# Kernel optimization log

Measured on AMD Instinct MI355X. Metric: run time of the kernel, lower is better.

Reference implementation:

```python
import jax, jax.numpy as jnp
import numpy as np

B, S, D, R, N_IN, N_PROC, K = 4, 4096, 1024, 128, 8, 32, 4

def setup_inputs() -> dict:
    key = jax.random.key(0)
    k1, k2, k3, k4, k5 = jax.random.split(key, 5)
    x = jax.random.normal(k1, (B, S, D), dtype=jnp.float32)
    input_weights = jax.random.uniform(k2, (B, S, N_IN), dtype=jnp.float32)
    process_indices = jax.random.randint(k3, (B, S, K), 0, N_PROC, dtype=jnp.int32)
    # params: orthogonal-ish init approximated by scaled gaussian
    input_neurons = jax.random.normal(k4, (N_IN, D, R), dtype=jnp.float32) / np.sqrt(D).astype(np.float32)
    process_neurons = jax.random.normal(k5, (N_PROC, R), dtype=jnp.float32)
    process_neurons = process_neurons / (jnp.linalg.norm(process_neurons, axis=-1, keepdims=True) + 1e-8)
    return {"x": x, "input_weights": input_weights, "process_indices": process_indices,
            "input_neurons": input_neurons, "process_neurons": process_neurons}

def reference(x, input_weights, process_indices, input_neurons, process_neurons):
    # soft routing over input neurons: project with all N_IN matrices, weight, sum
    all_proj = jnp.einsum('bsd,ndr->bsnr', x, input_neurons)      # [B,S,N_IN,R]
    y = jnp.einsum('bsnr,bsn->bsr', all_proj, input_weights)       # [B,S,R]
    # gather per-token Householder vectors: [B,S,K,R]
    selected_v = process_neurons[process_indices]
    # sequential chain of K Householder reflections via scan over the K axis
    def step(xc, v):
        # v: [B,S,R]
        v_norm_sq = jnp.sum(v * v, axis=-1, keepdims=True) + 1e-8
        vn = v / jnp.sqrt(v_norm_sq)
        vTx = jnp.sum(xc * vn, axis=-1, keepdims=True)
        return xc - 2.0 * vn * vTx, None
    out, _ = jax.lax.scan(step, y, jnp.moveaxis(selected_v, 2, 0))
    return out
```

## Files before the change

### kernel.cpp

```cpp
#include <hip/hip_runtime.h>
#include <hip/hip_bf16.h>
#include <stdint.h>

#define D_DIM 1024
#define R_DIM 128
#define NIN   8
#define M_TOT 16384

typedef unsigned short u16;
typedef __attribute__((ext_vector_type(4))) float f32x4;
typedef __attribute__((ext_vector_type(8))) __bf16 bf16x8;

__device__ __forceinline__ u16 f2b(float f) {
    union { float f; uint32_t u; } v; v.f = f;
    uint32_t r = (v.u + 0x7FFFu + ((v.u >> 16) & 1u)) >> 16;
    return (u16)r;
}

__device__ __forceinline__ void gload16(const void* g, void* l) {
    __builtin_amdgcn_global_load_lds(
        (const __attribute__((address_space(1))) uint32_t*)g,
        (__attribute__((address_space(3))) uint32_t*)l, 16, 0, 0);
}

#define SBAR do { asm volatile("" ::: "memory"); __builtin_amdgcn_s_barrier(); asm volatile("" ::: "memory"); } while (0)
#define WVM4 asm volatile("s_waitcnt vmcnt(4)" ::: "memory")

__global__ __launch_bounds__(256)
void prep(const float* __restrict__ x, u16* __restrict__ xb,
          const float* __restrict__ inn, u16* __restrict__ Bt2) {
    if (blockIdx.x < 8192) {
        const size_t i = ((size_t)blockIdx.x * 256 + threadIdx.x) * 8;
        const f32x4 v0 = *(const f32x4*)&x[i];
        const f32x4 v1 = *(const f32x4*)&x[i + 4];
        union { u16 s[8]; uint4 v; } u;
#pragma unroll
        for (int q = 0; q < 4; ++q) { u.s[q] = f2b(v0[q]); u.s[4 + q] = f2b(v1[q]); }
        *(uint4*)&xb[i] = u.v;
    } else {
        const int idx = (int)blockIdx.x - 8192;
        const int n  = idx >> 4;
        const int d0 = (idx & 15) * 64;
        const int r   = threadIdx.x & 127;
        const int hf  = threadIdx.x >> 7;
        const size_t C = (size_t)((r >> 4) * 128 + n * 16 + (r & 15));
#pragma unroll
        for (int g = 0; g < 4; ++g) {
            const int gg = hf * 4 + g;
            union { u16 s[8]; uint4 v; } u;
#pragma unroll
            for (int jj = 0; jj < 8; ++jj)
                u.s[jj] = f2b(inn[((size_t)n * D_DIM + d0 + gg * 8 + jj) * R_DIM + r]);
            *(uint4*)&Bt2[C * D_DIM + d0 + gg * 8] = u.v;
        }
    }
}

__global__ __launch_bounds__(512, 2)
void gemm8(const u16* __restrict__ xb, const u16* __restrict__ Bt2,
           const float* __restrict__ iw, float* __restrict__ y) {
    __shared__ __align__(16) char smem[131072];
    char* As = smem;
    char* Bs = smem + 65536;

    const int tid  = threadIdx.x;
    const int wid  = tid >> 6, lane = tid & 63;
    const int wm = wid >> 2, wn = wid & 3;
    const int l15 = lane & 15, lq = lane >> 4;

    int wg = (int)blockIdx.x;
    wg = (wg & 7) * 32 + (wg >> 3);
    const int by = wg & 3, bx = wg >> 2;
    const int m0 = bx * 256, c0 = by * 256;

    const int sxor = ((tid & 7) * 16) ^ (((tid >> 3) & 7) << 4);
    const char* gA = (const char*)xb  + ((size_t)(m0 + (tid >> 3))) * 2048 + sxor;
    const char* gB = (const char*)Bt2 + ((size_t)(c0 + (tid >> 3))) * 2048 + sxor;

#define STA(T1, NB, Q) gload16(gA + (size_t)(Q) * 64 * 2048 + (size_t)(T1) * 128, As + (NB) * 32768 + (Q) * 8192 + tid * 16)
#define STB(T1, NB, C) gload16(gB + (size_t)(C) * 64 * 2048 + (size_t)(T1) * 128, Bs + (NB) * 32768 + (C) * 8192 + tid * 16)

#define RDA(DST, MH, CUR) \
    _Pragma("unroll") for (int i = 0; i < 4; ++i) \
    _Pragma("unroll") for (int kk = 0; kk < 2; ++kk) { \
        const int row = wm * 128 + (MH) * 64 + i * 16 + l15; \
        uint32_t off = (uint32_t)((CUR) * 32768 + row * 128 + kk * 64 + lq * 16); \
        off ^= (uint32_t)((row & 7) << 4); \
        DST[i][kk] = *(const bf16x8*)(As + off); }

#define RDB(NS, CUR) \
    _Pragma("unroll") for (int j = 0; j < 2; ++j) \
    _Pragma("unroll") for (int kk = 0; kk < 2; ++kk) { \
        const int cc = (NS) * 128 + wn * 32 + j * 16 + l15; \
        uint32_t off = (uint32_t)((CUR) * 32768 + cc * 128 + kk * 64 + lq * 16); \
        off ^= (uint32_t)((cc & 7) << 4); \
        b[NS][j][kk] = *(const bf16x8*)(Bs + off); }

#define MM(MH, NS, AF) do { \
    __builtin_amdgcn_s_setprio(1); \
    _Pragma("unroll") for (int i = 0; i < 4; ++i) \
    _Pragma("unroll") for (int j = 0; j < 2; ++j) \
    _Pragma("unroll") for (int kk = 0; kk < 2; ++kk) \
        acc[MH][NS][i][j] = __builtin_amdgcn_mfma_f32_16x16x32_bf16(AF[i][kk], b[NS][j][kk], acc[MH][NS][i][j], 0, 0, 0); \
    __builtin_amdgcn_s_setprio(0); } while (0)

    f32x4 acc[2][2][4][2] = {};

    STA(0, 0, 0); STA(0, 0, 2);
    STB(0, 0, 0); STB(0, 0, 1);
    STB(0, 0, 2); STB(0, 0, 3);
    STA(0, 0, 1); STA(0, 0, 3);
    WVM4; SBAR;

    for (int t = 0; t < 16; ++t) {
        const int cur = t & 1, nb = cur ^ 1;
        const int t1 = t + 1;
        const bool st = (t1 < 16);
        bf16x8 a0[4][2], a1[4][2], b[2][2][2];

        RDA(a0, 0, cur);
        RDB(0, cur);
        if (st) { STA(t1, nb, 0); STA(t1, nb, 2); }
        SBAR;
        MM(0, 0, a0);
        WVM4; SBAR;

        RDB(1, cur);
        if (st) { STB(t1, nb, 0); STB(t1, nb, 1); }
        SBAR;
        MM(0, 1, a0);
        WVM4; SBAR;

        RDA(a1, 1, cur);
        if (st) { STB(t1, nb, 2); STB(t1, nb, 3); }
        SBAR;
        MM(1, 0, a1);
        SBAR;

        if (st) { STA(t1, nb, 1); STA(t1, nb, 3); }
        SBAR;
        MM(1, 1, a1);
        WVM4; SBAR;
    }

    float* P0 = (float*)smem;
    float* P1 = (float*)(smem + 34816);
    const float* wrow = iw + (size_t)m0 * NIN;

    float own[2][2][4][4];
#pragma unroll
    for (int mh = 0; mh < 2; ++mh)
#pragma unroll
        for (int i = 0; i < 4; ++i)
#pragma unroll
            for (int e = 0; e < 4; ++e) {
                const int row = wm * 128 + mh * 64 + i * 16 + lq * 4 + e;
                const float w0 = wrow[row * NIN + wn * 2 + 0];
                const float w1 = wrow[row * NIN + wn * 2 + 1];
#pragma unroll
                for (int ns = 0; ns < 2; ++ns)
                    own[mh][ns][i][e] = w0 * acc[mh][ns][i][0][e] + w1 * acc[mh][ns][i][1][e];
            }

#define PIX(NS, ROW) ((NS) * (256 * 17) + (ROW) * 17 + l15)
    if (wn == 1 || wn == 3) {
        float* P = (wn == 1) ? P0 : P1;
#pragma unroll
        for (int mh = 0; mh < 2; ++mh)
#pragma unroll
            for (int ns = 0; ns < 2; ++ns)
#pragma unroll
                for (int i = 0; i < 4; ++i)
#pragma unroll
                    for (int e = 0; e < 4; ++e) {
                        const int row = wm * 128 + mh * 64 + i * 16 + lq * 4 + e;
                        P[PIX(ns, row)] = own[mh][ns][i][e];
                    }
    }
    SBAR;
    if (wn == 2) {
#pragma unroll
        for (int mh = 0; mh < 2; ++mh)
#pragma unroll
            for (int ns = 0; ns < 2; ++ns)
#pragma unroll
                for (int i = 0; i < 4; ++i)
#pragma unroll
                    for (int e = 0; e < 4; ++e) {
                        const int row = wm * 128 + mh * 64 + i * 16 + lq * 4 + e;
                        P1[PIX(ns, row)] += own[mh][ns][i][e];
                    }
    }
    SBAR;
    if (wn == 0) {
#pragma unroll
        for (int mh = 0; mh < 2; ++mh)
#pragma unroll
            for (int ns = 0; ns < 2; ++ns)
#pragma unroll
                for (int i = 0; i < 4; ++i)
#pragma unroll
                    for (int e = 0; e < 4; ++e) {
                        const int row = wm * 128 + mh * 64 + i * 16 + lq * 4 + e;
                        const float s = own[mh][ns][i][e] + P0[PIX(ns, row)] + P1[PIX(ns, row)];
                        y[(size_t)(m0 + row) * R_DIM + (2 * by + ns) * 16 + l15] = s;
                    }
    }
#undef PIX
#undef MM
#undef RDB
#undef RDA
#undef STB
#undef STA
}

__global__ __launch_bounds__(512)
void house(float* __restrict__ y, const int* __restrict__ pidx,
           const float* __restrict__ pn) {
    const int tid = threadIdx.x;
    const int row = tid >> 3;
    const int cg  = tid & 7;
    const int c0  = cg * 16;
    const int tok = blockIdx.x * 64 + row;

    float yv[16];
#pragma unroll
    for (int q = 0; q < 4; ++q) {
        const f32x4 s = *(const f32x4*)&y[(size_t)tok * R_DIM + c0 + q * 4];
        yv[q * 4 + 0] = s[0]; yv[q * 4 + 1] = s[1]; yv[q * 4 + 2] = s[2]; yv[q * 4 + 3] = s[3];
    }

    const int4 idx4 = *(const int4*)&pidx[tok * 4];
    const int idxs[4] = { idx4.x, idx4.y, idx4.z, idx4.w };

#pragma unroll
    for (int k = 0; k < 4; ++k) {
        const float* vptr = &pn[(size_t)idxs[k] * R_DIM + c0];
        float v[16];
#pragma unroll
        for (int q = 0; q < 4; ++q) {
            const f32x4 vv4 = *(const f32x4*)&vptr[q * 4];
            v[q * 4 + 0] = vv4[0]; v[q * 4 + 1] = vv4[1];
            v[q * 4 + 2] = vv4[2]; v[q * 4 + 3] = vv4[3];
        }
        float vy = 0.f, vv = 0.f;
#pragma unroll
        for (int j = 0; j < 16; ++j) { vy += v[j] * yv[j]; vv += v[j] * v[j]; }
#pragma unroll
        for (int o = 1; o < 8; o <<= 1) {
            vy += __shfl_xor(vy, o);
            vv += __shfl_xor(vv, o);
        }
        const float s = 2.0f * vy / (vv + 1e-8f);
#pragma unroll
        for (int j = 0; j < 16; ++j) yv[j] -= s * v[j];
    }

#pragma unroll
    for (int q = 0; q < 4; ++q) {
        f32x4 o; o[0] = yv[q*4+0]; o[1] = yv[q*4+1]; o[2] = yv[q*4+2]; o[3] = yv[q*4+3];
        *(f32x4*)&y[(size_t)tok * R_DIM + c0 + q * 4] = o;
    }
}

extern "C" void kernel_launch(void* const* d_in, const int* in_sizes, int n_in,
                              void* d_out, int out_size, void* d_ws, size_t ws_size,
                              hipStream_t stream) {
    const float* x   = (const float*)d_in[0];
    const float* iw  = (const float*)d_in[1];
    const int*   pix = (const int*)d_in[2];
    const float* inn = (const float*)d_in[3];
    const float* pn  = (const float*)d_in[4];
    float* out = (float*)d_out;

    u16* xb  = (u16*)d_ws;
    u16* Bt2 = (u16*)((char*)d_ws + (size_t)(32 << 20));

    prep<<<8320, 256, 0, stream>>>(x, xb, inn, Bt2);
    gemm8<<<256, 512, 0, stream>>>(xb, Bt2, iw, out);
    house<<<256, 512, 0, stream>>>(out, pix, pn);
}
```

Measured before the change: 66.35 us.

## Fuse x fp32-to-bf16 conversion into GEMM A-tile loading

Removes the separate prep pass that converted x to bf16 in a workspace. The GEMM now loads fp32 x straight into registers, converts it, and writes the swizzled bf16 tile into LDS, with the pipeline rescheduled around the new waits. This avoids writing and re-reading a 32MB intermediate, but doubles the A-side global bytes each GEMM block reads and adds register pressure and conversion work inside the main loop.

```diff
diff --git a/kernel.cpp b/kernel.cpp
--- a/kernel.cpp
+++ b/kernel.cpp
@@ -23,41 +23,31 @@
         (__attribute__((address_space(3))) uint32_t*)l, 16, 0, 0);
 }
 
-#define SBAR do { asm volatile("" ::: "memory"); __builtin_amdgcn_s_barrier(); asm volatile("" ::: "memory"); } while (0)
-#define WVM4 asm volatile("s_waitcnt vmcnt(4)" ::: "memory")
+#define SBAR  do { asm volatile("" ::: "memory"); __builtin_amdgcn_s_barrier(); asm volatile("" ::: "memory"); } while (0)
+#define SBARL do { asm volatile("s_waitcnt lgkmcnt(0)" ::: "memory"); __builtin_amdgcn_s_barrier(); asm volatile("" ::: "memory"); } while (0)
+#define WVMC(N) asm volatile("s_waitcnt vmcnt(" #N ")" ::: "memory")
 
 __global__ __launch_bounds__(256)
-void prep(const float* __restrict__ x, u16* __restrict__ xb,
-          const float* __restrict__ inn, u16* __restrict__ Bt2) {
-    if (blockIdx.x < 8192) {
-        const size_t i = ((size_t)blockIdx.x * 256 + threadIdx.x) * 8;
-        const f32x4 v0 = *(const f32x4*)&x[i];
-        const f32x4 v1 = *(const f32x4*)&x[i + 4];
+void prep_b(const float* __restrict__ inn, u16* __restrict__ Bt2) {
+    const int idx = (int)blockIdx.x;
+    const int n  = idx >> 4;
+    const int d0 = (idx & 15) * 64;
+    const int r   = threadIdx.x & 127;
+    const int hf  = threadIdx.x >> 7;
+    const size_t C = (size_t)((r >> 4) * 128 + n * 16 + (r & 15));
+#pragma unroll
+    for (int g = 0; g < 4; ++g) {
+        const int gg = hf * 4 + g;
         union { u16 s[8]; uint4 v; } u;
 #pragma unroll
-        for (int q = 0; q < 4; ++q) { u.s[q] = f2b(v0[q]); u.s[4 + q] = f2b(v1[q]); }
-        *(uint4*)&xb[i] = u.v;
-    } else {
-        const int idx = (int)blockIdx.x - 8192;
-        const int n  = idx >> 4;
-        const int d0 = (idx & 15) * 64;
-        const int r   = threadIdx.x & 127;
-        const int hf  = threadIdx.x >> 7;
-        const size_t C = (size_t)((r >> 4) * 128 + n * 16 + (r & 15));
-#pragma unroll
-        for (int g = 0; g < 4; ++g) {
-            const int gg = hf * 4 + g;
-            union { u16 s[8]; uint4 v; } u;
-#pragma unroll
-            for (int jj = 0; jj < 8; ++jj)
-                u.s[jj] = f2b(inn[((size_t)n * D_DIM + d0 + gg * 8 + jj) * R_DIM + r]);
-            *(uint4*)&Bt2[C * D_DIM + d0 + gg * 8] = u.v;
-        }
+        for (int jj = 0; jj < 8; ++jj)
+            u.s[jj] = f2b(inn[((size_t)n * D_DIM + d0 + gg * 8 + jj) * R_DIM + r]);
+        *(uint4*)&Bt2[C * D_DIM + d0 + gg * 8] = u.v;
     }
 }
 
 __global__ __launch_bounds__(512, 2)
-void gemm8(const u16* __restrict__ xb, const u16* __restrict__ Bt2,
+void gemm8(const float* __restrict__ x, const u16* __restrict__ Bt2,
            const float* __restrict__ iw, float* __restrict__ y) {
     __shared__ __align__(16) char smem[131072];
     char* As = smem;
@@ -73,12 +63,33 @@
     const int by = wg & 3, bx = wg >> 2;
     const int m0 = bx * 256, c0 = by * 256;
 
+    const int arow = tid >> 3;
+    const int slot = tid & 7;
+    const uint32_t awoff = (uint32_t)(arow * 128 + ((slot * 16) ^ ((arow & 7) << 4)));
+    const float* pAq[4];
+#pragma unroll
+    for (int Q = 0; Q < 4; ++Q)
+        pAq[Q] = x + (size_t)(m0 + Q * 64 + arow) * D_DIM + slot * 8;
+
     const int sxor = ((tid & 7) * 16) ^ (((tid >> 3) & 7) << 4);
-    const char* gA = (const char*)xb  + ((size_t)(m0 + (tid >> 3))) * 2048 + sxor;
     const char* gB = (const char*)Bt2 + ((size_t)(c0 + (tid >> 3))) * 2048 + sxor;
 
-#define STA(T1, NB, Q) gload16(gA + (size_t)(Q) * 64 * 2048 + (size_t)(T1) * 128, As + (NB) * 32768 + (Q) * 8192 + tid * 16)
 #define STB(T1, NB, C) gload16(gB + (size_t)(C) * 64 * 2048 + (size_t)(T1) * 128, Bs + (NB) * 32768 + (C) * 8192 + tid * 16)
+
+#define LDAG(AR, T1) do { \
+    const size_t ko_ = (size_t)(T1) * 64; \
+    _Pragma("unroll") for (int Q = 0; Q < 4; ++Q) { \
+        AR[Q][0] = *(const f32x4*)(pAq[Q] + ko_); \
+        AR[Q][1] = *(const f32x4*)(pAq[Q] + ko_ + 4); } \
+} while (0)
+
+#define WRA(AR, NB) do { \
+    _Pragma("unroll") for (int Q = 0; Q < 4; ++Q) { \
+        bf16x8 v8_; \
+        _Pragma("unroll") for (int j = 0; j < 4; ++j) { \
+            v8_[j] = (__bf16)AR[Q][0][j]; v8_[4 + j] = (__bf16)AR[Q][1][j]; } \
+        *(bf16x8*)(As + (NB) * 32768 + Q * 8192 + awoff) = v8_; } \
+} while (0)
 
 #define RDA(DST, MH, CUR) \
     _Pragma("unroll") for (int i = 0; i < 4; ++i) \
@@ -104,43 +115,38 @@
         acc[MH][NS][i][j] = __builtin_amdgcn_mfma_f32_16x16x32_bf16(AF[i][kk], b[NS][j][kk], acc[MH][NS][i][j], 0, 0, 0); \
     __builtin_amdgcn_s_setprio(0); } while (0)
 
+#define TILE(T, CUR, NB) do { \
+    const int t1_ = (T) + 1; const bool st_ = (t1_ < 16); \
+    bf16x8 a0[4][2], a1[4][2], b[2][2][2]; \
+    f32x4 ar[4][2]; \
+    RDA(a0, 0, CUR); RDB(0, CUR); \
+    if (st_) LDAG(ar, t1_); \
+    SBAR; MM(0, 0, a0); \
+    if (st_) { WVMC(8); } else { WVMC(0); } \
+    SBAR; \
+    RDB(1, CUR); \
+    if (st_) { STB(t1_, NB, 0); STB(t1_, NB, 1); STB(t1_, NB, 2); STB(t1_, NB, 3); } \
+    SBAR; MM(0, 1, a0); SBAR; \
+    RDA(a1, 1, CUR); \
+    if (st_) WRA(ar, NB); \
+    SBARL; MM(1, 0, a1); SBAR; \
+    MM(1, 1, a1); WVMC(2); SBAR; \
+} while (0)
+
     f32x4 acc[2][2][4][2] = {};
 
-    STA(0, 0, 0); STA(0, 0, 2);
-    STB(0, 0, 0); STB(0, 0, 1);
-    STB(0, 0, 2); STB(0, 0, 3);
-    STA(0, 0, 1); STA(0, 0, 3);
-    WVM4; SBAR;
-
-    for (int t = 0; t < 16; ++t) {
-        const int cur = t & 1, nb = cur ^ 1;
-        const int t1 = t + 1;
-        const bool st = (t1 < 16);
-        bf16x8 a0[4][2], a1[4][2], b[2][2][2];
-
-        RDA(a0, 0, cur);
-        RDB(0, cur);
-        if (st) { STA(t1, nb, 0); STA(t1, nb, 2); }
-        SBAR;
-        MM(0, 0, a0);
-        WVM4; SBAR;
-
-        RDB(1, cur);
-        if (st) { STB(t1, nb, 0); STB(t1, nb, 1); }
-        SBAR;
-        MM(0, 1, a0);
-        WVM4; SBAR;
-
-        RDA(a1, 1, cur);
-        if (st) { STB(t1, nb, 2); STB(t1, nb, 3); }
-        SBAR;
-        MM(1, 0, a1);
-        SBAR;
-
-        if (st) { STA(t1, nb, 1); STA(t1, nb, 3); }
-        SBAR;
-        MM(1, 1, a1);
-        WVM4; SBAR;
+    {
+        f32x4 par[4][2];
+        LDAG(par, 0);
+        STB(0, 0, 0); STB(0, 0, 1); STB(0, 0, 2); STB(0, 0, 3);
+        WRA(par, 0);
+        WVMC(0);
+        SBARL;
+    }
+
+    for (int t = 0; t < 16; t += 2) {
+        TILE(t, 0, 1);
+        TILE(t + 1, 1, 0);
     }
 
     float* P0 = (float*)smem;
@@ -177,7 +183,7 @@
                         P[PIX(ns, row)] = own[mh][ns][i][e];
                     }
     }
-    SBAR;
+    SBARL;
     if (wn == 2) {
 #pragma unroll
         for (int mh = 0; mh < 2; ++mh)
@@ -191,7 +197,7 @@
                         P1[PIX(ns, row)] += own[mh][ns][i][e];
                     }
     }
-    SBAR;
+    SBARL;
     if (wn == 0) {
 #pragma unroll
         for (int mh = 0; mh < 2; ++mh)
@@ -207,11 +213,13 @@
                     }
     }
 #undef PIX
+#undef TILE
 #undef MM
 #undef RDB
 #undef RDA
+#undef WRA
+#undef LDAG
 #undef STB
-#undef STA
 }
 
 __global__ __launch_bounds__(512)
@@ -273,10 +281,9 @@
     const float* pn  = (const float*)d_in[4];
     float* out = (float*)d_out;
 
-    u16* xb  = (u16*)d_ws;
-    u16* Bt2 = (u16*)((char*)d_ws + (size_t)(32 << 20));
-
-    prep<<<8320, 256, 0, stream>>>(x, xb, inn, Bt2);
-    gemm8<<<256, 512, 0, stream>>>(xb, Bt2, iw, out);
+    u16* Bt2 = (u16*)d_ws;
+
+    prep_b<<<128, 256, 0, stream>>>(inn, Bt2);
+    gemm8<<<256, 512, 0, stream>>>(x, Bt2, iw, out);
     house<<<256, 512, 0, stream>>>(out, pix, pn);
 }
```

New measurement: 169.7 us. 156% more time.
